# Kernel tuning notes

Measured on AMD Instinct MI355X. Metric: run time of the kernel, lower is better.

Reference implementation:

```python
import jax, jax.numpy as jnp
import numpy as np

B, DIM, H, W = 8, 128, 112, 112
WSZ, K = 7, 9
D4 = DIM // 4


def setup_inputs() -> dict:
    key = jax.random.key(0)
    ks = jax.random.split(key, 8)
    w = lambda k, shape: jax.random.normal(k, shape, jnp.float32) * 0.05
    return {
        'x_in': jax.random.normal(ks[0], (B, DIM, H, W), jnp.float32),
        'f_w': w(ks[1], (D4, DIM)), 'f_b': jnp.zeros((D4,), jnp.float32),
        'f_gn_w': jnp.ones((D4,), jnp.float32), 'f_gn_b': jnp.zeros((D4,), jnp.float32),
        'p_w': w(ks[2], (DIM, D4)), 'p_b': jnp.zeros((DIM,), jnp.float32),
        'p_gn_w': jnp.ones((DIM,), jnp.float32), 'p_gn_b': jnp.zeros((DIM,), jnp.float32),
        'r_w': w(ks[3], (DIM, DIM)), 'r_b': jnp.zeros((DIM,), jnp.float32),
        'r_gn_w': jnp.ones((DIM,), jnp.float32), 'r_gn_b': jnp.zeros((DIM,), jnp.float32),
        'e1_w': w(ks[4], (D4, 2 * D4)), 'e1_b': jnp.zeros((D4,), jnp.float32),
        'e2_w': w(ks[5], (1, D4)), 'e2_b': jnp.zeros((1,), jnp.float32),
        'gamma': jnp.ones((1,), jnp.float32), 'beta': jnp.zeros((1,), jnp.float32),
    }


def conv1x1(x, w, b):
    # 1x1 conv == channel matmul. x: (B,C,H,W), w: (O,C)
    return jnp.einsum('bchw,oc->bohw', x, w) + b[None, :, None, None]


def gn1(x, w, b, eps=1e-5):
    # GroupNorm(1, C): normalize over (C,H,W) per sample
    mu = x.mean(axis=(1, 2, 3), keepdims=True)
    var = x.var(axis=(1, 2, 3), keepdims=True)
    xn = (x - mu) * jax.lax.rsqrt(var + eps)
    return xn * w[None, :, None, None] + b[None, :, None, None]


def reference(x_in, f_w, f_b, f_gn_w, f_gn_b, p_w, p_b, p_gn_w, p_gn_b,
              r_w, r_b, r_gn_w, r_gn_b, e1_w, e1_b, e2_w, e2_b, gamma, beta):
    b, c, h, w_ = x_in.shape
    wg = hg = WSZ
    pw, ph = h // wg, w_ // hg  # per-window spatial dims (16,16)

    residual = gn1(conv1x1(x_in, r_w, r_b), r_gn_w, r_gn_b)

    # 'b c (Wg w) (Hg h) -> (b Wg Hg) c w h'
    x = x_in.reshape(b, c, wg, pw, hg, ph).transpose(0, 2, 4, 1, 3, 5)
    x = x.reshape(b * wg * hg, c, pw, ph)

    f = gn1(conv1x1(x, f_w, f_b), f_gn_w, f_gn_b)  # (Bp, D4, pw, ph)
    bp, c4, hp, wp = f.shape
    n = hp * wp

    xf = f.reshape(bp, c4, n).transpose(0, 2, 1)  # (Bp, N, C4) nodes

    gy, gx = jnp.meshgrid(jnp.arange(hp), jnp.arange(wp), indexing='ij')
    grid = jnp.stack([gy, gx], axis=-1).astype(jnp.float32).reshape(n, 2)
    grid = (grid - grid.mean(0)) / (grid.std(0, ddof=1) + 1e-5)  # torch std is unbiased

    xa = jnp.concatenate([xf, jnp.broadcast_to(grid, (bp, n, 2))], axis=-1)
    xn = xa / jnp.maximum(jnp.linalg.norm(xa, axis=-1, keepdims=True), 1e-8)
    sim = jnp.einsum('bnd,bmd->bnm', xn, xn)  # (Bp, N, N) cosine sim
    sim = jnp.where(jnp.eye(n, dtype=bool), -jnp.inf, sim)
    _, topk_idx = jax.lax.top_k(sim, K)  # (Bp, N, K)

    # gather neighbor messages; scatter_add back to row == sum over K (rows are dense)
    msg = jax.vmap(lambda a, i: a[i])(xf, topk_idx)          # (Bp, N, K, C4)
    src = jnp.broadcast_to(xf[:, :, None, :], msg.shape)      # (Bp, N, K, C4)
    ef = jnp.concatenate([src, msg], axis=-1)                 # (Bp, N, K, 2*C4)
    h1 = jax.nn.silu(ef @ e1_w.T + e1_b)
    wgt = jax.nn.sigmoid(h1 @ e2_w.T + e2_b)[..., 0]          # (Bp, N, K)
    out = (msg * wgt[..., None]).sum(axis=2)                  # (Bp, N, C4)

    out = out * gamma + xf * beta
    out = out.reshape(bp, hp, wp, c4).transpose(0, 3, 1, 2)   # (Bp, C4, hp, wp)

    # '(b Wg Hg) c w h -> b c (Wg w) (Hg h)'
    out = out.reshape(b, wg, hg, c4, hp, wp).transpose(0, 3, 1, 4, 2, 5)
    out = out.reshape(b, c4, h, w_)

    out = gn1(conv1x1(out, p_w, p_b), p_gn_w, p_gn_b) + residual
    return out
```

## Files before the change

### kernel.cpp

```cpp
#include <hip/hip_runtime.h>
#include <hip/hip_fp16.h>
#include <math.h>

#define CIN 128
#define C4  32
#define HW  12544
#define NPIX 256
#define KNB 9
#define NWIN 392

__device__ inline double wave_sum(double v) {
#pragma unroll
    for (int off = 32; off; off >>= 1) v += __shfl_down(v, off);
    return v;
}

#define TOP9_INSERT(sv, mi, tv, ti)                                  \
    {                                                                \
        _Pragma("unroll")                                            \
        for (int j = KNB - 1; j >= 1; --j) {                         \
            bool cj  = (sv) > tv[j];                                 \
            bool cjm = (sv) > tv[j - 1];                             \
            tv[j] = cj ? (cjm ? tv[j - 1] : (sv)) : tv[j];           \
            ti[j] = cj ? (cjm ? ti[j - 1] : (mi)) : ti[j];           \
        }                                                            \
        bool c0 = (sv) > tv[0];                                      \
        tv[0] = c0 ? (sv) : tv[0];                                   \
        ti[0] = c0 ? (mi) : ti[0];                                   \
    }

__global__ __launch_bounds__(512, 2) void fconv_rstats_kernel(
    const float* __restrict__ x_in,
    const float* __restrict__ f_w, const float* __restrict__ f_b,
    const float* __restrict__ f_gn_w, const float* __restrict__ f_gn_b,
    const float* __restrict__ r_w, const float* __restrict__ r_b,
    float* __restrict__ xfws, double* __restrict__ invnws,
    double* __restrict__ stats)
{
    __shared__ __align__(16) char smem[34944];
    const int t = threadIdx.x;

    if (blockIdx.x < NWIN) {
        double* wbufd = (double*)smem;
        double* vbuf  = (double*)smem;
        double* red   = (double*)(smem + 34816);
        const int win = blockIdx.x;
        const int b = win / 49, wg = (win / 7) % 7, hg = win % 7;
        const int n = t & 255, s = t >> 8;
        const int py = n >> 4, px = n & 15;

        for (int i = t; i < C4 * CIN; i += 512) {
            int o = i >> 7, c = i & 127;
            wbufd[(c >> 1) * 64 + o * 2 + (c & 1)] = (double)f_w[i];
        }
        __syncthreads();

        const float* xb = x_in + (size_t)b * CIN * HW + (size_t)(wg * 16 + py) * 112 + (hg * 16 + px);
        double acc[16];
#pragma unroll
        for (int j = 0; j < 16; ++j) acc[j] = 0.0;
        {
            const double2* wrow = (const double2*)wbufd + 16 * s;
            for (int c2 = 0; c2 < 64; ++c2) {
                double xv0 = (double)xb[(size_t)(2 * c2) * HW];
                double xv1 = (double)xb[(size_t)(2 * c2 + 1) * HW];
                const double2* wr = wrow + c2 * 32;
#pragma unroll
                for (int j = 0; j < 16; ++j) {
                    double2 w2 = wr[j];
                    acc[j] = fma(w2.x, xv0, acc[j]);
                    acc[j] = fma(w2.y, xv1, acc[j]);
                }
            }
        }
        double s1 = 0.0, s2 = 0.0;
#pragma unroll
        for (int j = 0; j < 16; ++j) {
            double v = acc[j] + (double)f_b[16 * s + j];
            acc[j] = v; s1 += v; s2 += v * v;
        }
        s1 = wave_sum(s1); s2 = wave_sum(s2);
        {
            int w = t >> 6;
            if ((t & 63) == 0) { red[w] = s1; red[8 + w] = s2; }
        }
        __syncthreads();
        double rs1 = 0.0, rs2 = 0.0;
#pragma unroll
        for (int w = 0; w < 8; ++w) { rs1 += red[w]; rs2 += red[8 + w]; }
        const double mu   = rs1 * (1.0 / 8192.0);
        const double var  = rs2 * (1.0 / 8192.0) - mu * mu;
        const double rstd = 1.0 / sqrt(var + 1e-5);

        float myv[16];
#pragma unroll
        for (int j = 0; j < 16; ++j) {
            int c = 16 * s + j;
            myv[j] = (float)((acc[j] - mu) * rstd * (double)f_gn_w[c] + (double)f_gn_b[c]);
        }
        float* xrow = xfws + (size_t)(win * 256 + n) * 36;
#pragma unroll
        for (int q4 = 0; q4 < 4; ++q4) {
            float4 f = { myv[4 * q4], myv[4 * q4 + 1], myv[4 * q4 + 2], myv[4 * q4 + 3] };
            ((float4*)(xrow + 16 * s))[q4] = f;
        }
        const double ginv = 1.0 / (sqrt(5440.0 / 255.0) + 1e-5);
        const float gyf = (float)(((double)py - 7.5) * ginv);
        const float gxf = (float)(((double)px - 7.5) * ginv);
        if (s == 0) {
            float4 g4 = { gyf, gxf, 0.f, 0.f };
            ((float4*)(xrow + 32))[0] = g4;
        }
        if (s == 1) {
#pragma unroll
            for (int j = 0; j < 16; ++j) vbuf[n * 17 + j] = (double)myv[j];
        }
        __syncthreads();
        if (s == 0) {
            double nrm = 0.0;
#pragma unroll
            for (int j = 0; j < 16; ++j) { double x = (double)myv[j]; nrm += x * x; }
#pragma unroll
            for (int j = 0; j < 16; ++j) { double x = vbuf[n * 17 + j]; nrm += x * x; }
            double xg = (double)gyf; nrm += xg * xg;
            double xh = (double)gxf; nrm += xh * xh;
            invnws[win * 256 + n] = 1.0 / fmax(sqrt(nrm), 1e-8);
        }
    } else {
        float*  wt  = (float*)smem;
        double* red = (double*)(smem + 34816);
        const int idx = blockIdx.x - NWIN;
        const int b = idx / 98, rem = idx % 98;
        const int oc = rem / 49, pg = rem % 49;
        const int sh = t >> 8, n = t & 255;
        for (int i = t; i < 64 * CIN; i += 512)
            wt[(i & 127) * 64 + (i >> 7)] = r_w[oc * 64 * CIN + i];
        __syncthreads();
        const float* xb = x_in + (size_t)b * CIN * HW + pg * 256 + n;
        float acc[32];
#pragma unroll
        for (int o = 0; o < 32; ++o) acc[o] = r_b[oc * 64 + sh * 32 + o];
        for (int c0 = 0; c0 < CIN; c0 += 8) {
            float xv[8];
#pragma unroll
            for (int u = 0; u < 8; ++u) xv[u] = xb[(size_t)(c0 + u) * HW];
#pragma unroll
            for (int u = 0; u < 8; ++u)
#pragma unroll
                for (int o = 0; o < 32; ++o)
                    acc[o] = fmaf(wt[(c0 + u) * 64 + sh * 32 + o], xv[u], acc[o]);
        }
        double s1 = 0.0, s2 = 0.0;
#pragma unroll
        for (int o = 0; o < 32; ++o) { double v = (double)acc[o]; s1 += v; s2 += v * v; }
        s1 = wave_sum(s1); s2 = wave_sum(s2);
        {
            int w = t >> 6;
            if ((t & 63) == 0) { red[w] = s1; red[8 + w] = s2; }
        }
        __syncthreads();
        if (t == 0) {
            double a = 0.0, c = 0.0;
#pragma unroll
            for (int w = 0; w < 8; ++w) { a += red[w]; c += red[8 + w]; }
            atomicAdd(&stats[b * 4 + 0], a);
            atomicAdd(&stats[b * 4 + 1], c);
        }
    }
}

__global__ __launch_bounds__(256, 4) void sim_kernel(
    const float* __restrict__ xfws, const double* __restrict__ invnws,
    float* __restrict__ pval, short* __restrict__ pidx)
{
    __shared__ __align__(16) float xfm[64 * 36];
    __shared__ double invm[64];
    const int bid = blockIdx.x;
    const int win = bid >> 2, m0 = (bid & 3) << 6;
    const int n = threadIdx.x;

    const float* src = xfws + (size_t)(win * 256 + m0) * 36;
    for (int i = n; i < 64 * 36; i += 256) xfm[i] = src[i];
    if (n < 64) invm[n] = invnws[win * 256 + m0 + n];

    double xad[36];
    {
        const float4* own = (const float4*)(xfws + (size_t)(win * 256 + n) * 36);
#pragma unroll
        for (int q = 0; q < 9; ++q) {
            float4 f = own[q];
            xad[q * 4 + 0] = (double)f.x; xad[q * 4 + 1] = (double)f.y;
            xad[q * 4 + 2] = (double)f.z; xad[q * 4 + 3] = (double)f.w;
        }
    }
    const double inv_self = invnws[win * 256 + n];
    __syncthreads();

    float tv[KNB]; int ti[KNB];
#pragma unroll
    for (int k = 0; k < KNB; ++k) { tv[k] = -INFINITY; ti[k] = 0; }
#pragma unroll 2
    for (int mm = 0; mm < 64; ++mm) {
        const int m = m0 + mm;
        const float4* xm = (const float4*)(xfm + mm * 36);
        double d0 = 0.0, d1 = 0.0, d2 = 0.0, d3 = 0.0;
#pragma unroll
        for (int q = 0; q < 9; ++q) {
            float4 f = xm[q];
            d0 = fma((double)f.x, xad[q * 4 + 0], d0);
            d1 = fma((double)f.y, xad[q * 4 + 1], d1);
            d2 = fma((double)f.z, xad[q * 4 + 2], d2);
            d3 = fma((double)f.w, xad[q * 4 + 3], d3);
        }
        double d = (d0 + d1) + (d2 + d3);
        float sv = (float)(d * (inv_self * invm[mm]));
        sv = (m == n) ? -INFINITY : sv;
        TOP9_INSERT(sv, m, tv, ti);
    }
    const size_t base = ((size_t)bid * 256 + n) * 9;
#pragma unroll
    for (int k = 0; k < KNB; ++k) { pval[base + k] = tv[k]; pidx[base + k] = (short)ti[k]; }
}

__global__ __launch_bounds__(512, 2) void merge_mlp_kernel(
    const float* __restrict__ xfws,
    const float* __restrict__ pval, const short* __restrict__ pidx,
    const float* __restrict__ e1_w, const float* __restrict__ e1_b,
    const float* __restrict__ e2_w, const float* __restrict__ e2_b,
    const float* __restrict__ gamma, const float* __restrict__ beta,
    const float* __restrict__ p_w, const float* __restrict__ p_b,
    float* __restrict__ gnn, double* __restrict__ stats)
{
    __shared__ __align__(16) char smem[80640];
    float*   xf    = (float*)smem;
    __half2* hm2   = (__half2*)(smem + 37888);
    float*   hs    = (float*)(smem + 55296);
    float*   e1w   = (float*)(smem + 72192);
    short*   Ti    = (short*)(smem + 72192);
    float*   Wt    = (float*)(smem + 75520);
    float*   e2w_s = (float*)(smem + 80384);
    double*  red   = (double*)(smem + 80512);
    float*   pwt   = (float*)smem;
    float*   gnx   = (float*)(smem + 55296);

    const int bid  = blockIdx.x;
    const int win  = bid >> 1, half = bid & 1;
    const int b = win / 49, wg = (win / 7) % 7, hg = win % 7;
    const int t = threadIdx.x;
    const int nl = t & 127, s = t >> 7;
    const int gn = half * 128 + nl;

    {
        const float* src = xfws + (size_t)win * 256 * 36;
        for (int i = t; i < 9216; i += 512) xf[(i / 36) * 37 + (i % 36)] = src[i];
        for (int i = t; i < 2048; i += 512) e1w[i] = e1_w[i];
        if (t < C4) e2w_s[t] = e2_w[t];
    }
    __syncthreads();

    {
        float xr[C4];
#pragma unroll
        for (int c = 0; c < C4; ++c) xr[c] = xf[gn * 37 + c];
        const int j0 = 8 * s;
#pragma unroll
        for (int jj = 0; jj < 8; ++jj) {
            const int j = j0 + jj;
            float h0 = e1_b[j], h1 = 0.f;
#pragma unroll
            for (int c = 0; c < C4; c += 2) {
                h0 = fmaf(e1w[j * 64 + c], xr[c], h0);
                h1 = fmaf(e1w[j * 64 + c + 1], xr[c + 1], h1);
            }
            hs[nl * 33 + j] = h0 + h1;
        }
    }
    {
        const int mh = t & 255, jh = t >> 8;
        float xr[C4];
#pragma unroll
        for (int c = 0; c < C4; ++c) xr[c] = xf[mh * 37 + c];
        const int j0 = 16 * jh;
#pragma unroll
        for (int u = 0; u < 8; ++u) {
            const int j = j0 + 2 * u;
            float a0 = 0.f, a1 = 0.f;
#pragma unroll
            for (int c = 0; c < C4; ++c) {
                a0 = fmaf(e1w[j * 64 + 32 + c], xr[c], a0);
                a1 = fmaf(e1w[(j + 1) * 64 + 32 + c], xr[c], a1);
            }
            hm2[mh * 17 + 8 * jh + u] = __floats2half2_rn(a0, a1);
        }
    }
    __syncthreads();

    if (s == 0) {
        float tv[KNB]; int ti[KNB];
#pragma unroll
        for (int k = 0; k < KNB; ++k) { tv[k] = -INFINITY; ti[k] = 0; }
        for (int qd = 0; qd < 4; ++qd) {
            const size_t base = ((size_t)(win * 4 + qd) * 256 + gn) * 9;
#pragma unroll
            for (int k = 0; k < KNB; ++k) {
                float sv = pval[base + k];
                int   mi = (int)pidx[base + k];
                TOP9_INSERT(sv, mi, tv, ti);
            }
        }
#pragma unroll
        for (int k = 0; k < KNB; ++k) Ti[nl * 9 + k] = (short)ti[k];
    }
    __syncthreads();

    {
        float hsr[C4];
#pragma unroll
        for (int c = 0; c < C4; ++c) hsr[c] = hs[nl * 33 + c];
        const float e2b = e2_b[0];
        for (int k = s; k < KNB; k += 4) {
            const int m = (int)Ti[nl * 9 + k];
            float a2 = 0.f;
#pragma unroll
            for (int jp = 0; jp < 16; ++jp) {
                float2 hv = __half22float2(hm2[m * 17 + jp]);
                float h0 = hsr[2 * jp] + hv.x;
                float h1 = hsr[2 * jp + 1] + hv.y;
                float sg0 = 1.f / (1.f + __expf(-h0));
                a2 = fmaf(e2w_s[2 * jp], h0 * sg0, a2);
                float sg1 = 1.f / (1.f + __expf(-h1));
                a2 = fmaf(e2w_s[2 * jp + 1], h1 * sg1, a2);
            }
            Wt[nl * 9 + k] = 1.f / (1.f + __expf(-(a2 + e2b)));
        }
    }
    __syncthreads();

    {
        short tis[KNB]; float wks[KNB];
#pragma unroll
        for (int k = 0; k < KNB; ++k) { tis[k] = Ti[nl * 9 + k]; wks[k] = Wt[nl * 9 + k]; }
        const float g = gamma[0], be = beta[0];
        const int py = gn >> 4, px = gn & 15;
        float* gp = gnn + (size_t)b * C4 * HW + (size_t)(wg * 16 + py) * 112 + (hg * 16 + px);
        const int c0 = 8 * s;
#pragma unroll
        for (int cc = 0; cc < 8; ++cc) {
            const int c = c0 + cc;
            float o = 0.f;
#pragma unroll
            for (int k = 0; k < KNB; ++k)
                o = fmaf(wks[k], xf[(int)tis[k] * 37 + c], o);
            float gl = fmaf(g, o, be * xf[gn * 37 + c]);
            gp[(size_t)c * HW] = gl;
            gnx[nl * 33 + c] = gl;
        }
    }
    __syncthreads();

    for (int i = t; i < 4096; i += 512) pwt[(i & 31) * 128 + (i >> 5)] = p_w[i];
    __syncthreads();
    {
        float gr[C4];
#pragma unroll
        for (int c = 0; c < C4; ++c) gr[c] = gnx[nl * 33 + c];
        const int o0 = 32 * s;
        double s1 = 0.0, s2 = 0.0;
        for (int o = 0; o < 32; ++o) {
            float a = p_b[o0 + o];
#pragma unroll
            for (int c = 0; c < C4; ++c) a = fmaf(pwt[c * 128 + o0 + o], gr[c], a);
            s1 += (double)a; s2 += (double)a * (double)a;
        }
        s1 = wave_sum(s1); s2 = wave_sum(s2);
        int w = t >> 6;
        if ((t & 63) == 0) { red[w] = s1; red[8 + w] = s2; }
    }
    __syncthreads();
    if (t == 0) {
        double a = 0.0, c = 0.0;
#pragma unroll
        for (int w = 0; w < 8; ++w) { a += red[w]; c += red[8 + w]; }
        atomicAdd(&stats[b * 4 + 2], a);
        atomicAdd(&stats[b * 4 + 3], c);
    }
}

__global__ __launch_bounds__(256, 4) void final_kernel(
    const float* __restrict__ x_in, const float* __restrict__ gnn,
    const float* __restrict__ r_w, const float* __restrict__ r_b,
    const float* __restrict__ r_gn_w, const float* __restrict__ r_gn_b,
    const float* __restrict__ p_w, const float* __restrict__ p_b,
    const float* __restrict__ p_gn_w, const float* __restrict__ p_gn_b,
    const double* __restrict__ stats,
    float* __restrict__ out)
{
    __shared__ float rwt[32 * CIN];
    __shared__ float pwt[32 * C4];
    const int idx = blockIdx.x;
    const int b = idx / 196, rem = idx % 196;
    const int ocq = rem / 49, pg = rem % 49;
    const int t = threadIdx.x;

    for (int i = t; i < 32 * CIN; i += 256)
        rwt[(i & 127) * 32 + (i >> 7)] = r_w[(size_t)(ocq * 32) * CIN + i];
    for (int i = t; i < 32 * C4; i += 256)
        pwt[(i & 31) * 32 + (i >> 5)] = p_w[(size_t)(ocq * 32) * C4 + i];
    __syncthreads();

    const double NN = (double)CIN * HW;
    const double mu_r = stats[b * 4 + 0] / NN;
    const float  rs_r = (float)(1.0 / sqrt(stats[b * 4 + 1] / NN - mu_r * mu_r + 1e-5));
    const double mu_p = stats[b * 4 + 2] / NN;
    const float  rs_p = (float)(1.0 / sqrt(stats[b * 4 + 3] / NN - mu_p * mu_p + 1e-5));
    const float fmur = (float)mu_r, fmup = (float)mu_p;

    const int p = pg * 256 + t;
    const float* xb = x_in + (size_t)b * CIN * HW + p;
    const float* gb = gnn + (size_t)b * C4 * HW + p;
    float* ob = out + (size_t)b * CIN * HW + p;

    float xg[C4];
#pragma unroll
    for (int c = 0; c < C4; ++c) xg[c] = gb[(size_t)c * HW];

    float accR[32], accP[32];
#pragma unroll
    for (int o = 0; o < 32; ++o) {
        accR[o] = r_b[ocq * 32 + o];
        accP[o] = p_b[ocq * 32 + o];
    }
    for (int c0 = 0; c0 < CIN; c0 += 8) {
        float xv[8];
#pragma unroll
        for (int u = 0; u < 8; ++u) xv[u] = xb[(size_t)(c0 + u) * HW];
#pragma unroll
        for (int u = 0; u < 8; ++u)
#pragma unroll
            for (int o = 0; o < 32; ++o)
                accR[o] = fmaf(rwt[(c0 + u) * 32 + o], xv[u], accR[o]);
    }
#pragma unroll
    for (int c = 0; c < C4; ++c)
#pragma unroll
        for (int o = 0; o < 32; ++o)
            accP[o] = fmaf(pwt[c * 32 + o], xg[c], accP[o]);

#pragma unroll
    for (int o = 0; o < 32; ++o) {
        const int O = ocq * 32 + o;
        float yr = (accR[o] - fmur) * rs_r * r_gn_w[O] + r_gn_b[O];
        float yp = (accP[o] - fmup) * rs_p * p_gn_w[O] + p_gn_b[O];
        ob[(size_t)O * HW] = yp + yr;
    }
}

extern "C" void kernel_launch(void* const* d_in, const int* in_sizes, int n_in,
                              void* d_out, int out_size, void* d_ws, size_t ws_size,
                              hipStream_t stream)
{
    const float* x_in   = (const float*)d_in[0];
    const float* f_w    = (const float*)d_in[1];
    const float* f_b    = (const float*)d_in[2];
    const float* f_gn_w = (const float*)d_in[3];
    const float* f_gn_b = (const float*)d_in[4];
    const float* p_w    = (const float*)d_in[5];
    const float* p_b    = (const float*)d_in[6];
    const float* p_gn_w = (const float*)d_in[7];
    const float* p_gn_b = (const float*)d_in[8];
    const float* r_w    = (const float*)d_in[9];
    const float* r_b    = (const float*)d_in[10];
    const float* r_gn_w = (const float*)d_in[11];
    const float* r_gn_b = (const float*)d_in[12];
    const float* e1_w   = (const float*)d_in[13];
    const float* e1_b   = (const float*)d_in[14];
    const float* e2_w   = (const float*)d_in[15];
    const float* e2_b   = (const float*)d_in[16];
    const float* gamma  = (const float*)d_in[17];
    const float* beta   = (const float*)d_in[18];

    char* wsb = (char*)d_ws;
    float*  gnn    = (float*) (wsb + 0);
    double* stats  = (double*)(wsb + 12845056);
    float*  xfws   = (float*) (wsb + 12845312);
    double* invnws = (double*)(wsb + 27296000);
    float*  pval   = (float*) (wsb + 28098816);
    short*  pidx   = (short*) (wsb + 42549504);

    hipMemsetAsync(stats, 0, 32 * sizeof(double), stream);
    fconv_rstats_kernel<<<NWIN + 784, 512, 0, stream>>>(
        x_in, f_w, f_b, f_gn_w, f_gn_b, r_w, r_b, xfws, invnws, stats);
    sim_kernel<<<NWIN * 4, 256, 0, stream>>>(xfws, invnws, pval, pidx);
    merge_mlp_kernel<<<NWIN * 2, 512, 0, stream>>>(
        xfws, pval, pidx, e1_w, e1_b, e2_w, e2_b, gamma, beta, p_w, p_b, gnn, stats);
    final_kernel<<<1568, 256, 0, stream>>>(
        x_in, gnn, r_w, r_b, r_gn_w, r_gn_b, p_w, p_b, p_gn_w, p_gn_b, stats, (float*)d_out);
}
```

Before: 408.0 us.

## Pre-transpose weights once and read them via scalar loads instead of LDS staging

Adds a prep kernel that transposes f_w (to double), r_w and p_w into workspace once. The kernels then drop their per-block shared-memory weight staging and barriers and read weights directly from global memory, using readfirstlane so the addresses are wave-uniform and can go through scalar loads. The similarity kernel reads neighbour features from global instead of LDS and skips the zero padding channels. This trades LDS traffic and sync for scalar-cache dependence and an extra kernel launch.

```diff
diff --git a/kernel.cpp b/kernel.cpp
--- a/kernel.cpp
+++ b/kernel.cpp
@@ -5,7 +5,6 @@
 #define CIN 128
 #define C4  32
 #define HW  12544
-#define NPIX 256
 #define KNB 9
 #define NWIN 392
 
@@ -29,54 +28,53 @@
         ti[0] = c0 ? (mi) : ti[0];                                   \
     }
 
+__global__ __launch_bounds__(256) void prep_kernel(
+    const float* __restrict__ f_w, const float* __restrict__ r_w,
+    const float* __restrict__ p_w,
+    double* __restrict__ fw64t, float* __restrict__ rwt_t, float* __restrict__ pwt_t)
+{
+    const int i = blockIdx.x * 256 + threadIdx.x;
+    if (i < 4096)  fw64t[(i & 127) * 32 + (i >> 7)]  = (double)f_w[i];
+    if (i < 16384) rwt_t[(i & 127) * 128 + (i >> 7)] = r_w[i];
+    if (i < 4096)  pwt_t[(i & 31) * 128 + (i >> 5)]  = p_w[i];
+}
+
 __global__ __launch_bounds__(512, 2) void fconv_rstats_kernel(
     const float* __restrict__ x_in,
-    const float* __restrict__ f_w, const float* __restrict__ f_b,
+    const double* __restrict__ fw64t, const float* __restrict__ f_b,
     const float* __restrict__ f_gn_w, const float* __restrict__ f_gn_b,
-    const float* __restrict__ r_w, const float* __restrict__ r_b,
+    const float* __restrict__ rwt_t, const float* __restrict__ r_b,
     float* __restrict__ xfws, double* __restrict__ invnws,
     double* __restrict__ stats)
 {
     __shared__ __align__(16) char smem[34944];
+    double* vbuf = (double*)smem;
+    double* red  = (double*)(smem + 34816);
     const int t = threadIdx.x;
 
     if (blockIdx.x < NWIN) {
-        double* wbufd = (double*)smem;
-        double* vbuf  = (double*)smem;
-        double* red   = (double*)(smem + 34816);
         const int win = blockIdx.x;
         const int b = win / 49, wg = (win / 7) % 7, hg = win % 7;
         const int n = t & 255, s = t >> 8;
         const int py = n >> 4, px = n & 15;
-
-        for (int i = t; i < C4 * CIN; i += 512) {
-            int o = i >> 7, c = i & 127;
-            wbufd[(c >> 1) * 64 + o * 2 + (c & 1)] = (double)f_w[i];
-        }
-        __syncthreads();
+        const int rs = __builtin_amdgcn_readfirstlane(s);
 
         const float* xb = x_in + (size_t)b * CIN * HW + (size_t)(wg * 16 + py) * 112 + (hg * 16 + px);
+        const double* wB = fw64t + 16 * rs;
         double acc[16];
 #pragma unroll
         for (int j = 0; j < 16; ++j) acc[j] = 0.0;
-        {
-            const double2* wrow = (const double2*)wbufd + 16 * s;
-            for (int c2 = 0; c2 < 64; ++c2) {
-                double xv0 = (double)xb[(size_t)(2 * c2) * HW];
-                double xv1 = (double)xb[(size_t)(2 * c2 + 1) * HW];
-                const double2* wr = wrow + c2 * 32;
-#pragma unroll
-                for (int j = 0; j < 16; ++j) {
-                    double2 w2 = wr[j];
-                    acc[j] = fma(w2.x, xv0, acc[j]);
-                    acc[j] = fma(w2.y, xv1, acc[j]);
-                }
-            }
+#pragma unroll 2
+        for (int c = 0; c < CIN; ++c) {
+            double xv = (double)xb[(size_t)c * HW];
+            const double* wr = wB + c * 32;
+#pragma unroll
+            for (int j = 0; j < 16; ++j) acc[j] = fma(wr[j], xv, acc[j]);
         }
         double s1 = 0.0, s2 = 0.0;
 #pragma unroll
         for (int j = 0; j < 16; ++j) {
-            double v = acc[j] + (double)f_b[16 * s + j];
+            double v = acc[j] + (double)f_b[16 * rs + j];
             acc[j] = v; s1 += v; s2 += v * v;
         }
         s1 = wave_sum(s1); s2 = wave_sum(s2);
@@ -95,14 +93,14 @@
         float myv[16];
 #pragma unroll
         for (int j = 0; j < 16; ++j) {
-            int c = 16 * s + j;
+            int c = 16 * rs + j;
             myv[j] = (float)((acc[j] - mu) * rstd * (double)f_gn_w[c] + (double)f_gn_b[c]);
         }
         float* xrow = xfws + (size_t)(win * 256 + n) * 36;
 #pragma unroll
         for (int q4 = 0; q4 < 4; ++q4) {
             float4 f = { myv[4 * q4], myv[4 * q4 + 1], myv[4 * q4 + 2], myv[4 * q4 + 3] };
-            ((float4*)(xrow + 16 * s))[q4] = f;
+            ((float4*)(xrow + 16 * rs))[q4] = f;
         }
         const double ginv = 1.0 / (sqrt(5440.0 / 255.0) + 1e-5);
         const float gyf = (float)(((double)py - 7.5) * ginv);
@@ -127,28 +125,22 @@
             invnws[win * 256 + n] = 1.0 / fmax(sqrt(nrm), 1e-8);
         }
     } else {
-        float*  wt  = (float*)smem;
-        double* red = (double*)(smem + 34816);
         const int idx = blockIdx.x - NWIN;
         const int b = idx / 98, rem = idx % 98;
         const int oc = rem / 49, pg = rem % 49;
         const int sh = t >> 8, n = t & 255;
-        for (int i = t; i < 64 * CIN; i += 512)
-            wt[(i & 127) * 64 + (i >> 7)] = r_w[oc * 64 * CIN + i];
-        __syncthreads();
+        const int rsh = __builtin_amdgcn_readfirstlane(sh);
+        const float* wR = rwt_t + oc * 64 + rsh * 32;
         const float* xb = x_in + (size_t)b * CIN * HW + pg * 256 + n;
         float acc[32];
 #pragma unroll
-        for (int o = 0; o < 32; ++o) acc[o] = r_b[oc * 64 + sh * 32 + o];
-        for (int c0 = 0; c0 < CIN; c0 += 8) {
-            float xv[8];
-#pragma unroll
-            for (int u = 0; u < 8; ++u) xv[u] = xb[(size_t)(c0 + u) * HW];
-#pragma unroll
-            for (int u = 0; u < 8; ++u)
-#pragma unroll
-                for (int o = 0; o < 32; ++o)
-                    acc[o] = fmaf(wt[(c0 + u) * 64 + sh * 32 + o], xv[u], acc[o]);
+        for (int o = 0; o < 32; ++o) acc[o] = r_b[oc * 64 + rsh * 32 + o];
+#pragma unroll 2
+        for (int c = 0; c < CIN; ++c) {
+            float xv = xb[(size_t)c * HW];
+            const float* wr = wR + c * 128;
+#pragma unroll
+            for (int o = 0; o < 32; ++o) acc[o] = fmaf(wr[o], xv, acc[o]);
         }
         double s1 = 0.0, s2 = 0.0;
 #pragma unroll
@@ -173,49 +165,46 @@
     const float* __restrict__ xfws, const double* __restrict__ invnws,
     float* __restrict__ pval, short* __restrict__ pidx)
 {
-    __shared__ __align__(16) float xfm[64 * 36];
-    __shared__ double invm[64];
     const int bid = blockIdx.x;
     const int win = bid >> 2, m0 = (bid & 3) << 6;
     const int n = threadIdx.x;
 
-    const float* src = xfws + (size_t)(win * 256 + m0) * 36;
-    for (int i = n; i < 64 * 36; i += 256) xfm[i] = src[i];
-    if (n < 64) invm[n] = invnws[win * 256 + m0 + n];
-
-    double xad[36];
+    double xad[34];
     {
         const float4* own = (const float4*)(xfws + (size_t)(win * 256 + n) * 36);
 #pragma unroll
-        for (int q = 0; q < 9; ++q) {
+        for (int q = 0; q < 8; ++q) {
             float4 f = own[q];
             xad[q * 4 + 0] = (double)f.x; xad[q * 4 + 1] = (double)f.y;
             xad[q * 4 + 2] = (double)f.z; xad[q * 4 + 3] = (double)f.w;
         }
-    }
-    const double inv_self = invnws[win * 256 + n];
-    __syncthreads();
+        float4 g = own[8];
+        xad[32] = (double)g.x; xad[33] = (double)g.y;
+    }
+    const double inv_self = invnws[(size_t)win * 256 + n];
+    const float*  xmb  = xfws + (size_t)(win * 256 + m0) * 36;
+    const double* invb = invnws + (size_t)win * 256 + m0;
 
     float tv[KNB]; int ti[KNB];
 #pragma unroll
     for (int k = 0; k < KNB; ++k) { tv[k] = -INFINITY; ti[k] = 0; }
 #pragma unroll 2
     for (int mm = 0; mm < 64; ++mm) {
-        const int m = m0 + mm;
-        const float4* xm = (const float4*)(xfm + mm * 36);
+        const float* xm = xmb + mm * 36;
         double d0 = 0.0, d1 = 0.0, d2 = 0.0, d3 = 0.0;
 #pragma unroll
-        for (int q = 0; q < 9; ++q) {
-            float4 f = xm[q];
-            d0 = fma((double)f.x, xad[q * 4 + 0], d0);
-            d1 = fma((double)f.y, xad[q * 4 + 1], d1);
-            d2 = fma((double)f.z, xad[q * 4 + 2], d2);
-            d3 = fma((double)f.w, xad[q * 4 + 3], d3);
-        }
+        for (int q = 0; q < 8; ++q) {
+            d0 = fma((double)xm[4 * q + 0], xad[4 * q + 0], d0);
+            d1 = fma((double)xm[4 * q + 1], xad[4 * q + 1], d1);
+            d2 = fma((double)xm[4 * q + 2], xad[4 * q + 2], d2);
+            d3 = fma((double)xm[4 * q + 3], xad[4 * q + 3], d3);
+        }
+        d0 = fma((double)xm[32], xad[32], d0);
+        d1 = fma((double)xm[33], xad[33], d1);
         double d = (d0 + d1) + (d2 + d3);
-        float sv = (float)(d * (inv_self * invm[mm]));
-        sv = (m == n) ? -INFINITY : sv;
-        TOP9_INSERT(sv, m, tv, ti);
+        float sv = (float)(d * (inv_self * invb[mm]));
+        sv = (m0 + mm == n) ? -INFINITY : sv;
+        TOP9_INSERT(sv, m0 + mm, tv, ti);
     }
     const size_t base = ((size_t)bid * 256 + n) * 9;
 #pragma unroll
@@ -228,73 +217,70 @@
     const float* __restrict__ e1_w, const float* __restrict__ e1_b,
     const float* __restrict__ e2_w, const float* __restrict__ e2_b,
     const float* __restrict__ gamma, const float* __restrict__ beta,
-    const float* __restrict__ p_w, const float* __restrict__ p_b,
+    const float* __restrict__ pwt_t, const float* __restrict__ p_b,
     float* __restrict__ gnn, double* __restrict__ stats)
 {
-    __shared__ __align__(16) char smem[80640];
-    float*   xf    = (float*)smem;
-    __half2* hm2   = (__half2*)(smem + 37888);
-    float*   hs    = (float*)(smem + 55296);
-    float*   e1w   = (float*)(smem + 72192);
-    short*   Ti    = (short*)(smem + 72192);
-    float*   Wt    = (float*)(smem + 75520);
-    float*   e2w_s = (float*)(smem + 80384);
-    double*  red   = (double*)(smem + 80512);
-    float*   pwt   = (float*)smem;
-    float*   gnx   = (float*)(smem + 55296);
-
-    const int bid  = blockIdx.x;
-    const int win  = bid >> 1, half = bid & 1;
+    __shared__ __align__(16) char smem[75136];
+    float*   xf  = (float*)smem;
+    __half2* hm2 = (__half2*)(smem + 33792);
+    float*   hs  = (float*)(smem + 51200);
+    float*   gnx = (float*)(smem + 51200);
+    short*   Ti  = (short*)(smem + 68096);
+    float*   Wt  = (float*)(smem + 70400);
+    double*  red = (double*)(smem + 75008);
+
+    const int bid = blockIdx.x;
+    const int win = bid >> 1, half = bid & 1;
     const int b = win / 49, wg = (win / 7) % 7, hg = win % 7;
     const int t = threadIdx.x;
     const int nl = t & 127, s = t >> 7;
     const int gn = half * 128 + nl;
+    const int rs = __builtin_amdgcn_readfirstlane(s);
 
     {
         const float* src = xfws + (size_t)win * 256 * 36;
-        for (int i = t; i < 9216; i += 512) xf[(i / 36) * 37 + (i % 36)] = src[i];
-        for (int i = t; i < 2048; i += 512) e1w[i] = e1_w[i];
-        if (t < C4) e2w_s[t] = e2_w[t];
+        for (int i = t; i < 8192; i += 512)
+            xf[(i >> 5) * 33 + (i & 31)] = src[(i >> 5) * 36 + (i & 31)];
     }
     __syncthreads();
 
     {
         float xr[C4];
 #pragma unroll
-        for (int c = 0; c < C4; ++c) xr[c] = xf[gn * 37 + c];
-        const int j0 = 8 * s;
+        for (int c = 0; c < C4; ++c) xr[c] = xf[gn * 33 + c];
 #pragma unroll
         for (int jj = 0; jj < 8; ++jj) {
-            const int j = j0 + jj;
+            const int j = 8 * rs + jj;
+            const float* w = e1_w + j * 64;
             float h0 = e1_b[j], h1 = 0.f;
 #pragma unroll
             for (int c = 0; c < C4; c += 2) {
-                h0 = fmaf(e1w[j * 64 + c], xr[c], h0);
-                h1 = fmaf(e1w[j * 64 + c + 1], xr[c + 1], h1);
+                h0 = fmaf(w[c], xr[c], h0);
+                h1 = fmaf(w[c + 1], xr[c + 1], h1);
             }
             hs[nl * 33 + j] = h0 + h1;
         }
     }
     {
-        const int mh = t & 255, jh = t >> 8;
+        const int mh = t & 255;
+        const int rjh = __builtin_amdgcn_readfirstlane(t >> 8);
         float xr[C4];
 #pragma unroll
-        for (int c = 0; c < C4; ++c) xr[c] = xf[mh * 37 + c];
-        const int j0 = 16 * jh;
+        for (int c = 0; c < C4; ++c) xr[c] = xf[mh * 33 + c];
 #pragma unroll
         for (int u = 0; u < 8; ++u) {
-            const int j = j0 + 2 * u;
+            const int j = 16 * rjh + 2 * u;
+            const float* w0 = e1_w + j * 64 + 32;
+            const float* w1 = e1_w + (j + 1) * 64 + 32;
             float a0 = 0.f, a1 = 0.f;
 #pragma unroll
             for (int c = 0; c < C4; ++c) {
-                a0 = fmaf(e1w[j * 64 + 32 + c], xr[c], a0);
-                a1 = fmaf(e1w[(j + 1) * 64 + 32 + c], xr[c], a1);
+                a0 = fmaf(w0[c], xr[c], a0);
+                a1 = fmaf(w1[c], xr[c], a1);
             }
-            hm2[mh * 17 + 8 * jh + u] = __floats2half2_rn(a0, a1);
-        }
-    }
-    __syncthreads();
-
+            hm2[mh * 17 + 8 * rjh + u] = __floats2half2_rn(a0, a1);
+        }
+    }
     if (s == 0) {
         float tv[KNB]; int ti[KNB];
 #pragma unroll
@@ -327,9 +313,9 @@
                 float h0 = hsr[2 * jp] + hv.x;
                 float h1 = hsr[2 * jp + 1] + hv.y;
                 float sg0 = 1.f / (1.f + __expf(-h0));
-                a2 = fmaf(e2w_s[2 * jp], h0 * sg0, a2);
+                a2 = fmaf(e2_w[2 * jp], h0 * sg0, a2);
                 float sg1 = 1.f / (1.f + __expf(-h1));
-                a2 = fmaf(e2w_s[2 * jp + 1], h1 * sg1, a2);
+                a2 = fmaf(e2_w[2 * jp + 1], h1 * sg1, a2);
             }
             Wt[nl * 9 + k] = 1.f / (1.f + __expf(-(a2 + e2b)));
         }
@@ -343,35 +329,37 @@
         const float g = gamma[0], be = beta[0];
         const int py = gn >> 4, px = gn & 15;
         float* gp = gnn + (size_t)b * C4 * HW + (size_t)(wg * 16 + py) * 112 + (hg * 16 + px);
-        const int c0 = 8 * s;
 #pragma unroll
         for (int cc = 0; cc < 8; ++cc) {
-            const int c = c0 + cc;
+            const int c = 8 * rs + cc;
             float o = 0.f;
 #pragma unroll
             for (int k = 0; k < KNB; ++k)
-                o = fmaf(wks[k], xf[(int)tis[k] * 37 + c], o);
-            float gl = fmaf(g, o, be * xf[gn * 37 + c]);
+                o = fmaf(wks[k], xf[(int)tis[k] * 33 + c], o);
+            float gl = fmaf(g, o, be * xf[gn * 33 + c]);
             gp[(size_t)c * HW] = gl;
             gnx[nl * 33 + c] = gl;
         }
     }
     __syncthreads();
 
-    for (int i = t; i < 4096; i += 512) pwt[(i & 31) * 128 + (i >> 5)] = p_w[i];
-    __syncthreads();
     {
         float gr[C4];
 #pragma unroll
         for (int c = 0; c < C4; ++c) gr[c] = gnx[nl * 33 + c];
-        const int o0 = 32 * s;
+        const int o0 = 32 * rs;
+        float a[32];
+#pragma unroll
+        for (int o = 0; o < 32; ++o) a[o] = p_b[o0 + o];
+#pragma unroll 2
+        for (int c = 0; c < C4; ++c) {
+            const float* w = pwt_t + c * 128 + o0;
+#pragma unroll
+            for (int o = 0; o < 32; ++o) a[o] = fmaf(w[o], gr[c], a[o]);
+        }
         double s1 = 0.0, s2 = 0.0;
-        for (int o = 0; o < 32; ++o) {
-            float a = p_b[o0 + o];
-#pragma unroll
-            for (int c = 0; c < C4; ++c) a = fmaf(pwt[c * 128 + o0 + o], gr[c], a);
-            s1 += (double)a; s2 += (double)a * (double)a;
-        }
+#pragma unroll
+        for (int o = 0; o < 32; ++o) { double v = (double)a[o]; s1 += v; s2 += v * v; }
         s1 = wave_sum(s1); s2 = wave_sum(s2);
         int w = t >> 6;
         if ((t & 63) == 0) { red[w] = s1; red[8 + w] = s2; }
@@ -386,27 +374,19 @@
     }
 }
 
-__global__ __launch_bounds__(256, 4) void final_kernel(
+__global__ __launch_bounds__(256) void final_kernel(
     const float* __restrict__ x_in, const float* __restrict__ gnn,
-    const float* __restrict__ r_w, const float* __restrict__ r_b,
+    const float* __restrict__ rwt_t, const float* __restrict__ r_b,
     const float* __restrict__ r_gn_w, const float* __restrict__ r_gn_b,
-    const float* __restrict__ p_w, const float* __restrict__ p_b,
+    const float* __restrict__ pwt_t, const float* __restrict__ p_b,
     const float* __restrict__ p_gn_w, const float* __restrict__ p_gn_b,
     const double* __restrict__ stats,
     float* __restrict__ out)
 {
-    __shared__ float rwt[32 * CIN];
-    __shared__ float pwt[32 * C4];
     const int idx = blockIdx.x;
     const int b = idx / 196, rem = idx % 196;
     const int ocq = rem / 49, pg = rem % 49;
     const int t = threadIdx.x;
-
-    for (int i = t; i < 32 * CIN; i += 256)
-        rwt[(i & 127) * 32 + (i >> 7)] = r_w[(size_t)(ocq * 32) * CIN + i];
-    for (int i = t; i < 32 * C4; i += 256)
-        pwt[(i & 31) * 32 + (i >> 5)] = p_w[(size_t)(ocq * 32) * C4 + i];
-    __syncthreads();
 
     const double NN = (double)CIN * HW;
     const double mu_r = stats[b * 4 + 0] / NN;
@@ -430,22 +410,19 @@
         accR[o] = r_b[ocq * 32 + o];
         accP[o] = p_b[ocq * 32 + o];
     }
-    for (int c0 = 0; c0 < CIN; c0 += 8) {
-        float xv[8];
-#pragma unroll
-        for (int u = 0; u < 8; ++u) xv[u] = xb[(size_t)(c0 + u) * HW];
-#pragma unroll
-        for (int u = 0; u < 8; ++u)
-#pragma unroll
-            for (int o = 0; o < 32; ++o)
-                accR[o] = fmaf(rwt[(c0 + u) * 32 + o], xv[u], accR[o]);
-    }
-#pragma unroll
-    for (int c = 0; c < C4; ++c)
-#pragma unroll
-        for (int o = 0; o < 32; ++o)
-            accP[o] = fmaf(pwt[c * 32 + o], xg[c], accP[o]);
-
+#pragma unroll 2
+    for (int c = 0; c < CIN; ++c) {
+        float xv = xb[(size_t)c * HW];
+        const float* w = rwt_t + c * 128 + ocq * 32;
+#pragma unroll
+        for (int o = 0; o < 32; ++o) accR[o] = fmaf(w[o], xv, accR[o]);
+    }
+#pragma unroll
+    for (int c = 0; c < C4; ++c) {
+        const float* w = pwt_t + c * 128 + ocq * 32;
+#pragma unroll
+        for (int o = 0; o < 32; ++o) accP[o] = fmaf(w[o], xg[c], accP[o]);
+    }
 #pragma unroll
     for (int o = 0; o < 32; ++o) {
         const int O = ocq * 32 + o;
@@ -486,13 +463,17 @@
     double* invnws = (double*)(wsb + 27296000);
     float*  pval   = (float*) (wsb + 28098816);
     short*  pidx   = (short*) (wsb + 42549504);
+    double* fw64t  = (double*)(wsb + 49774848);
+    float*  rwt_t  = (float*) (wsb + 49807616);
+    float*  pwt_t  = (float*) (wsb + 49873152);
 
     hipMemsetAsync(stats, 0, 32 * sizeof(double), stream);
+    prep_kernel<<<64, 256, 0, stream>>>(f_w, r_w, p_w, fw64t, rwt_t, pwt_t);
     fconv_rstats_kernel<<<NWIN + 784, 512, 0, stream>>>(
-        x_in, f_w, f_b, f_gn_w, f_gn_b, r_w, r_b, xfws, invnws, stats);
+        x_in, fw64t, f_b, f_gn_w, f_gn_b, rwt_t, r_b, xfws, invnws, stats);
     sim_kernel<<<NWIN * 4, 256, 0, stream>>>(xfws, invnws, pval, pidx);
     merge_mlp_kernel<<<NWIN * 2, 512, 0, stream>>>(
-        xfws, pval, pidx, e1_w, e1_b, e2_w, e2_b, gamma, beta, p_w, p_b, gnn, stats);
+        xfws, pval, pidx, e1_w, e1_b, e2_w, e2_b, gamma, beta, pwt_t, p_b, gnn, stats);
     final_kernel<<<1568, 256, 0, stream>>>(
-        x_in, gnn, r_w, r_b, r_gn_w, r_gn_b, p_w, p_b, p_gn_w, p_gn_b, stats, (float*)d_out);
-}
+        x_in, gnn, rwt_t, r_b, r_gn_w, r_gn_b, pwt_t, p_b, p_gn_w, p_gn_b, stats, (float*)d_out);
+}
```

After: 327.1 us. -19.8%, faster.
